# Performance work log

Hardware: AMD Instinct MI355X
Metric: run time of the kernel (lower is better)

The kernel has to match this reference:

```python
import jax, jax.numpy as jnp
import numpy as np

N_NODES = 40000
N_EDGES = 640000
FEAT_IN = 128
EDGE_FEAT_IN = 16
HID = 128
N_LAYERS = 4
NUM_GRAPHS = 256


def _linear_params(key, fan_in, fan_out):
    k1, k2 = jax.random.split(key)
    s = 1.0 / np.sqrt(fan_in)
    W = jax.random.uniform(k1, (fan_in, fan_out), jnp.float32, -s, s)
    b = jax.random.uniform(k2, (fan_out,), jnp.float32, -s, s)
    return W, b


def setup_inputs() -> dict:
    key = jax.random.key(0)
    ks = jax.random.split(key, 8)
    h = jax.random.normal(ks[0], (N_NODES, FEAT_IN), jnp.float32)
    e = jax.random.normal(ks[1], (N_EDGES, EDGE_FEAT_IN), jnp.float32)
    edge_index = jax.random.randint(ks[2], (2, N_EDGES), 0, N_NODES, jnp.int32)
    batch = jnp.sort(jax.random.randint(ks[3], (N_NODES,), 0, NUM_GRAPHS, jnp.int32))

    W_embed, b_embed = _linear_params(ks[4], FEAT_IN, HID)
    W_eembed, b_eembed = _linear_params(ks[5], EDGE_FEAT_IN, HID)

    layer_keys = jax.random.split(ks[6], N_LAYERS * 3)
    Wm_l, bm_l, Wh_l, bh_l, We_l, be_l = [], [], [], [], [], []
    for i in range(N_LAYERS):
        Wm, bm = _linear_params(layer_keys[3 * i + 0], 3 * HID, HID)
        Wh, bh = _linear_params(layer_keys[3 * i + 1], 2 * HID, HID)
        We, be = _linear_params(layer_keys[3 * i + 2], 3 * HID, HID)
        Wm_l.append(Wm); bm_l.append(bm)
        Wh_l.append(Wh); bh_l.append(bh)
        We_l.append(We); be_l.append(be)

    return {
        "h": h, "e": e, "edge_index": edge_index, "batch": batch,
        "W_embed": W_embed, "b_embed": b_embed,
        "W_eembed": W_eembed, "b_eembed": b_eembed,
        "Wm": jnp.stack(Wm_l), "bm": jnp.stack(bm_l),
        "Wh": jnp.stack(Wh_l), "bh": jnp.stack(bh_l),
        "We": jnp.stack(We_l), "be": jnp.stack(be_l),
    }


def reference(h, e, W_embed, b_embed, W_eembed, b_eembed,
              Wm, bm, Wh, bh, We, be, edge_index, batch):
    send, rec = edge_index[0], edge_index[1]
    h = h @ W_embed + b_embed          # [N, H]
    e = e @ W_eembed + b_eembed        # [E, H]

    def layer(carry, params):
        h, e = carry
        Wm_i, bm_i, Wh_i, bh_i, We_i, be_i = params
        h_send = h[send]               # [E, H] gather
        h_rec = h[rec]                 # [E, H] gather
        cat3 = jnp.concatenate([h_send, h_rec, e], axis=1)  # [E, 3H]
        messages = cat3 @ Wm_i + bm_i                        # [E, H]
        agg = jax.ops.segment_sum(messages, rec, num_segments=N_NODES)  # scatter_add
        h_new = jnp.concatenate([h, agg], axis=1) @ Wh_i + bh_i
        # NOTE: e_update uses h_send/h_rec from the OLD h, as in the source.
        e_new = cat3 @ We_i + be_i
        return (h_new, e_new), None

    (h, e), _ = jax.lax.scan(layer, (h, e), (Wm, bm, Wh, bh, We, be))
    return jax.ops.segment_sum(h, batch, num_segments=NUM_GRAPHS)  # global_add_pool
```

## Files before the change

kernel.cpp:

```cpp
#include <hip/hip_runtime.h>
#include <hip/hip_bf16.h>

#define NN 40000
#define NE 640000
#define NG 256
#define EW 48

typedef __attribute__((ext_vector_type(8))) short bf16x8;
typedef __attribute__((ext_vector_type(4))) float f32x4;

__device__ __forceinline__ unsigned f2b_u(float f){
  unsigned u = __builtin_bit_cast(unsigned, f);
  u += 0x7fffu + ((u >> 16) & 1u);
  return u >> 16;
}
__device__ __forceinline__ float b2f(unsigned short h){
  unsigned u = ((unsigned)h) << 16;
  return __builtin_bit_cast(float, u);
}
__device__ __forceinline__ unsigned scale_pk(unsigned u, float dg){
  float lo = __builtin_bit_cast(float, u << 16);
  float hi = __builtin_bit_cast(float, u & 0xffff0000u);
  return f2b_u(lo * dg) | (f2b_u(hi * dg) << 16);
}

#define LSTRIDE 147456

__global__ __launch_bounds__(256) void pack2_k(
    const float* __restrict__ Wembed, const float* __restrict__ Wh,
    const float* __restrict__ We, unsigned short* __restrict__ wt,
    unsigned short* __restrict__ wp)
{
  __shared__ float T[64][65];
  const int bx = blockIdx.x;
  const int tx = threadIdx.x & 63, ty = threadIdx.x >> 6;
  const float* src; unsigned short* dst; int rowbase, stride, koff, jt, kt;
  if (bx < 4){
    src = Wembed; dst = wt; rowbase = 0; stride = 128; koff = 0;
    kt = bx & 1; jt = bx >> 1;
  } else {
    const int q = bx - 4, l = q / 24, w = q % 24;
    unsigned short* base = wt + 16384 + (size_t)l * LSTRIDE;
    const float* wh = Wh + (size_t)l * 256 * 128;
    const float* we = We + (size_t)l * 384 * 128;
    if (w < 4){       src = wh; rowbase = 0;   dst = base;          stride = 640; koff = 0;   kt = w & 1;        jt = w >> 1; }
    else if (w < 12){ const int u = w - 4;  src = we; rowbase = 128; dst = base + 81920;  stride = 256; koff = 0;   kt = u & 3; jt = u >> 2; }
    else if (w < 16){ const int u = w - 12; src = we; rowbase = 0;   dst = base + 114688; stride = 256; koff = 0;   kt = u & 1; jt = u >> 1; }
    else if (w < 20){ const int u = w - 16; src = we; rowbase = 256; dst = base + 114688; stride = 256; koff = 128; kt = u & 1; jt = u >> 1; }
    else {            const int u = w - 20; src = wh; rowbase = 128; dst = wp + l * 16384; stride = 128; koff = 0; kt = u & 1; jt = u >> 1; }
  }
  const int k0 = kt * 64, j0 = jt * 64;
  #pragma unroll
  for (int rr = 0; rr < 16; ++rr){
    const int r = ty + rr * 4;
    T[r][tx] = src[(size_t)(rowbase + k0 + r) * 128 + j0 + tx];
  }
  __syncthreads();
  #pragma unroll
  for (int rr = 0; rr < 16; ++rr){
    const int j = ty + rr * 4;
    dst[(size_t)(j0 + j) * stride + koff + k0 + tx] = (unsigned short)f2b_u(T[tx][j]);
  }
}

__global__ __launch_bounds__(256, 2) void prodg_k(
    const float* __restrict__ Wm, const unsigned short* __restrict__ wp,
    unsigned short* __restrict__ wt)
{
  __shared__ unsigned short As[128 * 128];
  __shared__ unsigned short Bs[128 * 128];
  const int l = blockIdx.x / 3, pi = blockIdx.x % 3;
  const int rowoff = (pi == 0) ? 128 : (pi == 1) ? 0 : 256;
  const int poff   = (pi == 0) ? 128 : (pi == 1) ? 256 : 384;
  const float* Am = Wm + (size_t)l * 384 * 128 + (size_t)rowoff * 128;
  const unsigned short* Bt = wp + l * 16384;
  unsigned short* base = wt + 16384 + (size_t)l * LSTRIDE;

  const int tid = threadIdx.x;
  const int lane = tid & 63, wave = tid >> 6;
  const int qm = (wave & 1) << 6, qn = (wave >> 1) << 6;
  const int lr = lane & 15, lkc = lane >> 4;
  const int chunk = tid & 15, r0 = tid >> 4;
  f32x4 acc[4][4] = {};

  #pragma unroll
  for (int rr = 0; rr < 8; ++rr){
    const int r = r0 + rr * 16;
    const float* Af = Am + ((size_t)r << 7) + chunk * 8;
    const float4 f0 = *(const float4*)Af;
    const float4 f1 = *(const float4*)(Af + 4);
    uint4 va;
    va.x = f2b_u(f0.x) | (f2b_u(f0.y) << 16);
    va.y = f2b_u(f0.z) | (f2b_u(f0.w) << 16);
    va.z = f2b_u(f1.x) | (f2b_u(f1.y) << 16);
    va.w = f2b_u(f1.z) | (f2b_u(f1.w) << 16);
    *(uint4*)&As[r * 128 + ((chunk ^ (r & 7)) << 3)] = va;
    *(uint4*)&Bs[r * 128 + ((chunk ^ (r & 7)) << 3)] =
        *(const uint4*)(Bt + (size_t)r * 128 + chunk * 8);
  }
  __syncthreads();
  #pragma unroll
  for (int kk = 0; kk < 4; ++kk){
    const int kc = kk * 4 + lkc;
    bf16x8 af[4], bfr[4];
    #pragma unroll
    for (int mi = 0; mi < 4; ++mi){
      const int r = qm + mi * 16 + lr;
      af[mi] = *(const bf16x8*)&As[r * 128 + ((kc ^ (r & 7)) << 3)];
    }
    #pragma unroll
    for (int ni = 0; ni < 4; ++ni){
      const int r = qn + ni * 16 + lr;
      bfr[ni] = *(const bf16x8*)&Bs[r * 128 + ((kc ^ (r & 7)) << 3)];
    }
    #pragma unroll
    for (int mi = 0; mi < 4; ++mi)
      #pragma unroll
      for (int ni = 0; ni < 4; ++ni)
        acc[mi][ni] = __builtin_amdgcn_mfma_f32_16x16x32_bf16(af[mi], bfr[ni], acc[mi][ni], 0, 0, 0);
  }

  const int rbase = (lane >> 4) << 2;
  #pragma unroll
  for (int mi = 0; mi < 4; ++mi){
    #pragma unroll
    for (int r = 0; r < 4; ++r){
      const int gr = qm + mi * 16 + rbase + r;
      #pragma unroll
      for (int ni = 0; ni < 4; ++ni){
        const int col = qn + ni * 16 + lr;
        const unsigned short b = (unsigned short)f2b_u(acc[mi][ni][r]);
        base[(size_t)col * 640 + poff + gr] = b;
        if (pi == 2) base[(size_t)col * 640 + 512 + gr] = b;
      }
    }
  }
}

__global__ __launch_bounds__(1024, 1) void vec2b_k(
    const float* __restrict__ bm, const float* __restrict__ be,
    const unsigned short* __restrict__ wt, const unsigned short* __restrict__ wp,
    float* __restrict__ rw)
{
  __shared__ unsigned short s_wp[16384];
  __shared__ unsigned short s_m3[16384];
  __shared__ unsigned short s_w3[16384];
  __shared__ float c[128], cb[128];
  __shared__ float part_rw[128][8], part_cn[128][8];
  const int t = threadIdx.x;
  const int j = t >> 3, p = t & 7;
  if (t < 128) c[t] = 0.f;

  for (int l = 0; l < 4; ++l){
    const unsigned short* base = wt + 16384 + (size_t)l * LSTRIDE;
    ((uint4*)s_wp)[t]        = ((const uint4*)(wp + l * 16384))[t];
    ((uint4*)s_wp)[t + 1024] = ((const uint4*)(wp + l * 16384))[t + 1024];
    {
      const uint4* srcm = (const uint4*)(base + (size_t)j * 640 + 384);
      ((uint4*)(s_m3 + j * 128))[p * 2]     = srcm[p * 2];
      ((uint4*)(s_m3 + j * 128))[p * 2 + 1] = srcm[p * 2 + 1];
      const uint4* srcw = (const uint4*)(base + 114688 + (size_t)j * 256 + 128);
      ((uint4*)(s_w3 + j * 128))[p * 2]     = srcw[p * 2];
      ((uint4*)(s_w3 + j * 128))[p * 2 + 1] = srcw[p * 2 + 1];
    }
    if (t < 128) cb[t] = bm[l * 128 + t];
    __syncthreads();
    float prw = 0.f, pcn = 0.f;
    #pragma unroll
    for (int q = 0; q < 16; ++q){
      const int kk = p * 16 + q;
      prw += cb[kk] * b2f(s_wp[j * 128 + kk]) + c[kk] * b2f(s_m3[j * 128 + kk]);
      pcn += c[kk] * b2f(s_w3[j * 128 + kk]);
    }
    part_rw[j][p] = prw; part_cn[j][p] = pcn;
    __syncthreads();
    if (t < 128){
      float rwj = 0.f, cnj = be[l * 128 + t];
      #pragma unroll
      for (int i = 0; i < 8; ++i){ rwj += part_rw[t][i]; cnj += part_cn[t][i]; }
      rw[l * 128 + t] = rwj;
      __syncthreads();
      c[t] = cnj;
    } else {
      __syncthreads();
    }
    __syncthreads();
  }
}

struct YCfg {
  const void* A[5];
  const unsigned short* Bt;
  unsigned short* out0;
  const float* bias;
  const float* rv;
  int np;
  int bstride;
  int scale_mask;
};
struct GArgs { YCfg y[3]; };

template<int AT0>
__global__ __launch_bounds__(256, 2) void gemm_multi(
    GArgs ga, int M, const float* __restrict__ degf)
{
  __shared__ unsigned short As[128 * 128];
  __shared__ unsigned short Bs[128 * 128];
  const YCfg c = ga.y[blockIdx.y];
  const int tid = threadIdx.x;
  const int m0 = blockIdx.x * 128;
  const int lane = tid & 63, wave = tid >> 6;
  const int qm = (wave & 1) << 6, qn = (wave >> 1) << 6;
  const int lr = lane & 15, lkc = lane >> 4;
  const int chunk = tid & 15, r0 = tid >> 4;
  f32x4 acc[4][4] = {};

  for (int p = 0; p < c.np; ++p){
    if (p) __syncthreads();
    const unsigned short* Ab = (const unsigned short*)c.A[p];
    const bool scl = (c.scale_mask >> p) & 1;
    #pragma unroll
    for (int rr = 0; rr < 8; ++rr){
      const int r = r0 + rr * 16;
      const int gr = m0 + r;
      uint4 va = make_uint4(0u, 0u, 0u, 0u);
      if (gr < M){
        if (AT0 && p == 0){
          const float* Af = (const float*)c.A[0] + ((size_t)gr << 7) + chunk * 8;
          const float4 f0 = *(const float4*)Af;
          const float4 f1 = *(const float4*)(Af + 4);
          va.x = f2b_u(f0.x) | (f2b_u(f0.y) << 16);
          va.y = f2b_u(f0.z) | (f2b_u(f0.w) << 16);
          va.z = f2b_u(f1.x) | (f2b_u(f1.y) << 16);
          va.w = f2b_u(f1.z) | (f2b_u(f1.w) << 16);
        } else {
          va = *(const uint4*)(Ab + ((size_t)gr << 7) + chunk * 8);
          if (scl){
            const float dg = degf[gr];
            va.x = scale_pk(va.x, dg); va.y = scale_pk(va.y, dg);
            va.z = scale_pk(va.z, dg); va.w = scale_pk(va.w, dg);
          }
        }
      }
      *(uint4*)&As[r * 128 + ((chunk ^ (r & 7)) << 3)] = va;
      *(uint4*)&Bs[r * 128 + ((chunk ^ (r & 7)) << 3)] =
          *(const uint4*)(c.Bt + (size_t)r * c.bstride + p * 128 + chunk * 8);
    }
    __syncthreads();
    #pragma unroll
    for (int kk = 0; kk < 4; ++kk){
      const int kc = kk * 4 + lkc;
      bf16x8 af[4], bfr[4];
      #pragma unroll
      for (int mi = 0; mi < 4; ++mi){
        const int r = qm + mi * 16 + lr;
        af[mi] = *(const bf16x8*)&As[r * 128 + ((kc ^ (r & 7)) << 3)];
      }
      #pragma unroll
      for (int ni = 0; ni < 4; ++ni){
        const int r = qn + ni * 16 + lr;
        bfr[ni] = *(const bf16x8*)&Bs[r * 128 + ((kc ^ (r & 7)) << 3)];
      }
      #pragma unroll
      for (int mi = 0; mi < 4; ++mi)
        #pragma unroll
        for (int ni = 0; ni < 4; ++ni)
          acc[mi][ni] = __builtin_amdgcn_mfma_f32_16x16x32_bf16(af[mi], bfr[ni], acc[mi][ni], 0, 0, 0);
    }
  }

  const int rbase = (lane >> 4) << 2;
  #pragma unroll
  for (int mi = 0; mi < 4; ++mi){
    #pragma unroll
    for (int r = 0; r < 4; ++r){
      const int gr = m0 + qm + mi * 16 + rbase + r;
      if (gr >= M) continue;
      const size_t ro = (size_t)gr << 7;
      float dg = 0.f;
      if (c.rv) dg = degf[gr];
      #pragma unroll
      for (int ni = 0; ni < 4; ++ni){
        const int col = qn + ni * 16 + lr;
        float v = acc[mi][ni][r];
        if (c.bias) v += c.bias[col];
        if (c.rv)   v += dg * c.rv[col];
        c.out0[ro + col] = (unsigned short)f2b_u(v);
      }
    }
  }
}

__global__ void fill_ell_k(const int* __restrict__ rec, const int* __restrict__ send,
                           int* __restrict__ cnt, int* __restrict__ ell_s,
                           int* __restrict__ ell_e){
  const int i = blockIdx.x * 256 + threadIdx.x;
  if (i < NE){
    const int r = rec[i];
    const int k = atomicAdd(&cnt[r], 1);
    if (k < EW){
      ell_s[r * EW + k] = send[i];
      ell_e[r * EW + k] = i;
    }
  }
}

__global__ void aux_k(const int* __restrict__ cnt, float* __restrict__ degf,
                      const int* __restrict__ batch, int* __restrict__ gptr){
  const int b = blockIdx.x, t = threadIdx.x;
  if (b < 157){
    const int i = b * 256 + t;
    if (i < NN) degf[i] = (float)cnt[i];
  } else {
    if (t < NG){
      int lo = 0, hi = NN;
      while (lo < hi){
        const int mid = (lo + hi) >> 1;
        if (batch[mid] < t) lo = mid + 1; else hi = mid;
      }
      gptr[t] = lo;
      if (t == 0) gptr[NG] = NN;
    }
  }
}

__global__ __launch_bounds__(256) void sraw_s0_k(
    const int* __restrict__ cnt, const int* __restrict__ ell_e,
    const float* __restrict__ e_in, const float* __restrict__ W,
    const float* __restrict__ bias, unsigned short* __restrict__ TPS)
{
  __shared__ float sums[16][16];
  __shared__ float dgs[16];
  __shared__ float Ws[2048];
  __shared__ float bs[128];
  const int t = threadIdx.x;
  const int n0 = blockIdx.x * 16;
  for (int i = t; i < 2048; i += 256) Ws[i] = W[i];
  if (t < 128) bs[t] = bias[t];
  {
    const int a = t >> 4, c16 = t & 15;
    const int n = n0 + a;
    const int m0 = cnt[n];
    const int m = (m0 < EW) ? m0 : EW;
    const int* row = ell_e + n * EW;
    float acc = 0.f;
    int j = 0;
    for (; j + 2 <= m; j += 2){
      const int e0 = row[j], e1 = row[j + 1];
      acc += e_in[(size_t)e0 * 16 + c16] + e_in[(size_t)e1 * 16 + c16];
    }
    if (j < m) acc += e_in[(size_t)row[j] * 16 + c16];
    sums[a][c16] = acc;
    if (c16 == 0) dgs[a] = (float)m0;
  }
  __syncthreads();
  #pragma unroll
  for (int i = 0; i < 8; ++i){
    const int o = t + 256 * i;
    const int node = o >> 7, col = o & 127;
    float acc = dgs[node] * bs[col];
    #pragma unroll
    for (int k = 0; k < 16; ++k) acc += sums[node][k] * Ws[k * 128 + col];
    TPS[((size_t)(n0 + node) << 7) + col] = (unsigned short)f2b_u(acc);
  }
}

__global__ __launch_bounds__(256) void gather_k(
    const int* __restrict__ cnt, const int* __restrict__ ell_s,
    const unsigned short* __restrict__ hb, unsigned short* __restrict__ tb)
{
  const int n = blockIdx.x * 4 + (threadIdx.x >> 6);
  const int lane = threadIdx.x & 63;
  const int half = lane >> 5, l32 = lane & 31;
  const int mc = cnt[n];
  const int m = (mc < EW) ? mc : EW;
  const unsigned short* colp = hb + 4 * l32;
  const int myidx = (lane < m) ? ell_s[n * EW + lane] : 0;
  float a0 = 0.f, a1 = 0.f, a2 = 0.f, a3 = 0.f;
  int k = 0;
  for (; k + 16 <= m; k += 16){
    int s[8];
    #pragma unroll
    for (int u = 0; u < 8; ++u) s[u] = __shfl(myidx, k + 2 * u + half);
    uint2 v[8];
    #pragma unroll
    for (int u = 0; u < 8; ++u) v[u] = *(const uint2*)(colp + ((size_t)s[u] << 7));
    #pragma unroll
    for (int u = 0; u < 8; ++u){
      a0 += b2f((unsigned short)(v[u].x & 0xffffu));
      a1 += b2f((unsigned short)(v[u].x >> 16));
      a2 += b2f((unsigned short)(v[u].y & 0xffffu));
      a3 += b2f((unsigned short)(v[u].y >> 16));
    }
  }
  for (; k + 4 <= m; k += 4){
    const int s0 = __shfl(myidx, k + half);
    const int s1 = __shfl(myidx, k + 2 + half);
    const uint2 v0 = *(const uint2*)(colp + ((size_t)s0 << 7));
    const uint2 v1 = *(const uint2*)(colp + ((size_t)s1 << 7));
    a0 += b2f((unsigned short)(v0.x & 0xffffu)) + b2f((unsigned short)(v1.x & 0xffffu));
    a1 += b2f((unsigned short)(v0.x >> 16)) + b2f((unsigned short)(v1.x >> 16));
    a2 += b2f((unsigned short)(v0.y & 0xffffu)) + b2f((unsigned short)(v1.y & 0xffffu));
    a3 += b2f((unsigned short)(v0.y >> 16)) + b2f((unsigned short)(v1.y >> 16));
  }
  for (; k < m; k += 2){
    if (k + half < m){
      const int s = __shfl(myidx, k + half);
      const uint2 v = *(const uint2*)(colp + ((size_t)s << 7));
      a0 += b2f((unsigned short)(v.x & 0xffffu));
      a1 += b2f((unsigned short)(v.x >> 16));
      a2 += b2f((unsigned short)(v.y & 0xffffu));
      a3 += b2f((unsigned short)(v.y >> 16));
    }
  }
  a0 += __shfl_xor(a0, 32); a1 += __shfl_xor(a1, 32);
  a2 += __shfl_xor(a2, 32); a3 += __shfl_xor(a3, 32);
  if (half == 0){
    uint2 o;
    o.x = f2b_u(a0) | (f2b_u(a1) << 16);
    o.y = f2b_u(a2) | (f2b_u(a3) << 16);
    *(uint2*)(tb + ((size_t)n << 7) + 4 * l32) = o;
  }
}

__global__ void pool_k(const int* __restrict__ gptr, const unsigned short* __restrict__ hb,
                       float* __restrict__ out)
{
  const int g = blockIdx.x * 4 + (threadIdx.x >> 6);
  const int lane = threadIdx.x & 63;
  float a0 = 0.f, a1 = 0.f;
  for (int n = gptr[g]; n < gptr[g + 1]; ++n){
    const unsigned v = *(const unsigned*)(hb + ((size_t)n << 7) + 2 * lane);
    a0 += b2f((unsigned short)(v & 0xffffu));
    a1 += b2f((unsigned short)(v >> 16));
  }
  float2 r; r.x = a0; r.y = a1;
  *(float2*)(out + (size_t)g * 128 + 2 * lane) = r;
}

extern "C" void kernel_launch(void* const* d_in, const int* in_sizes, int n_in,
                              void* d_out, int out_size, void* d_ws, size_t ws_size,
                              hipStream_t stream)
{
  const float* h_in     = (const float*)d_in[0];
  const float* e_in     = (const float*)d_in[1];
  const int*   eidx     = (const int*)d_in[2];
  const int*   batch    = (const int*)d_in[3];
  const float* W_embed  = (const float*)d_in[4];
  const float* b_embed  = (const float*)d_in[5];
  const float* W_eembed = (const float*)d_in[6];
  const float* b_eembed = (const float*)d_in[7];
  const float* Wm       = (const float*)d_in[8];
  const float* bm       = (const float*)d_in[9];
  const float* Wh       = (const float*)d_in[10];
  const float* bh       = (const float*)d_in[11];
  const float* We       = (const float*)d_in[12];
  const float* be       = (const float*)d_in[13];
  const int* send = eidx;
  const int* rec  = eidx + NE;

  char* ws = (char*)d_ws;
  size_t off = 0;
  auto alloc = [&](size_t bytes) -> char* {
    char* p = ws + off;
    off = (off + bytes + 255) & ~(size_t)255;
    return p;
  };
  unsigned short* wt  = (unsigned short*)alloc((size_t)(16384 + 4 * LSTRIDE) * 2);
  unsigned short* wp  = (unsigned short*)alloc((size_t)4 * 16384 * 2);
  unsigned short* hA  = (unsigned short*)alloc((size_t)NN * 128 * 2);
  unsigned short* hB  = (unsigned short*)alloc((size_t)NN * 128 * 2);
  unsigned short* Q0  = (unsigned short*)alloc((size_t)NN * 128 * 2);
  unsigned short* Q1  = (unsigned short*)alloc((size_t)NN * 128 * 2);
  unsigned short* T0  = (unsigned short*)alloc((size_t)NN * 128 * 2);
  unsigned short* T1  = (unsigned short*)alloc((size_t)NN * 128 * 2);
  unsigned short* tb  = (unsigned short*)alloc((size_t)NN * 128 * 2);
  float* rw   = (float*)alloc((size_t)512 * 4);
  int* cnt    = (int*)alloc((size_t)NN * 4);
  float* degf = (float*)alloc((size_t)NN * 4);
  int* gptr   = (int*)alloc((size_t)(NG + 1) * 4);
  int* ell_s  = (int*)alloc((size_t)NN * EW * 4);
  int* ell_e  = (int*)tb;

  if (off > ws_size) return;

  const dim3 B256(256);

  pack2_k<<<dim3(100), B256, 0, stream>>>(W_embed, Wh, We, wt, wp);
  prodg_k<<<dim3(12), B256, 0, stream>>>(Wm, wp, wt);
  vec2b_k<<<dim3(1), dim3(1024), 0, stream>>>(bm, be, wt, wp, rw);

  hipMemsetAsync(cnt, 0, (size_t)NN * 4, stream);
  fill_ell_k<<<dim3(2500), B256, 0, stream>>>(rec, send, cnt, ell_s, ell_e);
  aux_k<<<dim3(158), B256, 0, stream>>>(cnt, degf, batch, gptr);
  sraw_s0_k<<<dim3(NN / 16), B256, 0, stream>>>(cnt, ell_e, e_in, W_eembed, b_eembed, T0);

  {
    GArgs ga = {};
    ga.y[0].A[0] = h_in; ga.y[0].Bt = wt; ga.y[0].out0 = hA;
    ga.y[0].bias = b_embed; ga.y[0].np = 1; ga.y[0].bstride = 128;
    ga.y[0].scale_mask = 0;
    gemm_multi<1><<<dim3(313, 1), B256, 0, stream>>>(ga, NN, degf);
  }

  unsigned short* hc = hA;  unsigned short* hn = hB;
  unsigned short* Qc = Q0;  unsigned short* Qn = Q1;
  unsigned short* Tc = T0;  unsigned short* Tn = T1;
  for (int l = 0; l < 4; ++l){
    const unsigned short* LB = wt + 16384 + (size_t)l * LSTRIDE;

    gather_k<<<dim3(NN / 4), B256, 0, stream>>>(cnt, ell_s, hc, tb);

    GArgs ga = {};
    YCfg& y0 = ga.y[0];
    y0.A[0] = hc; y0.A[1] = hc; y0.A[2] = tb; y0.A[3] = Tc; y0.A[4] = Qc;
    y0.Bt = LB; y0.out0 = hn; y0.bias = bh + l * 128; y0.rv = rw + l * 128;
    y0.np = (l == 0) ? 4 : 5;
    y0.bstride = 640; y0.scale_mask = (1 << 1) | (1 << 4);
    int ny = 1;
    if (l < 3){
      YCfg& y1 = ga.y[1];
      y1.A[0] = hc; y1.A[1] = Qc; y1.Bt = LB + 81920;
      y1.out0 = Qn; y1.np = (l == 0) ? 1 : 2; y1.bstride = 256; y1.scale_mask = 0;
      YCfg& y2 = ga.y[2];
      y2.A[0] = tb; y2.A[1] = Tc; y2.Bt = LB + 114688;
      y2.out0 = Tn; y2.np = 2; y2.bstride = 256; y2.scale_mask = 0;
      ny = 3;
    }
    gemm_multi<0><<<dim3(313, ny), B256, 0, stream>>>(ga, NN, degf);

    unsigned short* t2;
    t2 = hc; hc = hn; hn = t2;
    t2 = Qc; Qc = Qn; Qn = t2;
    t2 = Tc; Tc = Tn; Tn = t2;
  }

  pool_k<<<dim3(NG / 4), B256, 0, stream>>>(gptr, hc, (float*)d_out);
}
```

Baseline: 599.4 us.

## Pre-fragment weights and load B operands directly from global memory in GEMM

Adds a kernel that rearranges the packed bf16 weight matrices into an MFMA-fragment-friendly layout, one 16K-element block per K-slice. The GEMM then reads B fragments straight from global/L2 instead of staging them through shared memory. This halves LDS usage and raises launch bounds to allow four blocks per SM. The trade-off is that every wave re-reads the weight fragments from cache on each k-step, which adds global load latency inside the MFMA loop.

```diff
diff --git a/kernel.cpp b/kernel.cpp
--- a/kernel.cpp
+++ b/kernel.cpp
@@ -137,6 +137,26 @@
   }
 }
 
+__global__ void frag_k(const unsigned short* __restrict__ wt,
+                       unsigned short* __restrict__ wf)
+{
+  const int gp = blockIdx.y;
+  const int g = blockIdx.x * 256 + threadIdx.x;
+  const int kc = g >> 7, r = g & 127;
+  const unsigned short* src; unsigned short* dst; int bstride, p;
+  if (gp == 0){ src = wt; dst = wf; bstride = 128; p = 0; }
+  else {
+    const int q = gp - 1, l = q / 9, w = q % 9;
+    const unsigned short* sb = wt + 16384 + (size_t)l * LSTRIDE;
+    dst = wf + 16384 + (size_t)l * LSTRIDE + w * 16384;
+    if (w < 5){      src = sb;           bstride = 640; p = w; }
+    else if (w < 7){ src = sb + 81920;   bstride = 256; p = w - 5; }
+    else {           src = sb + 114688;  bstride = 256; p = w - 7; }
+  }
+  *(uint4*)(dst + (size_t)g * 8) =
+      *(const uint4*)(src + (size_t)r * bstride + p * 128 + kc * 8);
+}
+
 __global__ __launch_bounds__(1024, 1) void vec2b_k(
     const float* __restrict__ bm, const float* __restrict__ be,
     const unsigned short* __restrict__ wt, const unsigned short* __restrict__ wp,
@@ -190,22 +210,21 @@
 
 struct YCfg {
   const void* A[5];
-  const unsigned short* Bt;
+  int bo[5];
   unsigned short* out0;
   const float* bias;
   const float* rv;
   int np;
-  int bstride;
   int scale_mask;
 };
 struct GArgs { YCfg y[3]; };
 
 template<int AT0>
-__global__ __launch_bounds__(256, 2) void gemm_multi(
-    GArgs ga, int M, const float* __restrict__ degf)
+__global__ __launch_bounds__(256, 4) void gemm_multi(
+    GArgs ga, int M, const float* __restrict__ degf,
+    const unsigned short* __restrict__ wf)
 {
   __shared__ unsigned short As[128 * 128];
-  __shared__ unsigned short Bs[128 * 128];
   const YCfg c = ga.y[blockIdx.y];
   const int tid = threadIdx.x;
   const int m0 = blockIdx.x * 128;
@@ -243,23 +262,20 @@
         }
       }
       *(uint4*)&As[r * 128 + ((chunk ^ (r & 7)) << 3)] = va;
-      *(uint4*)&Bs[r * 128 + ((chunk ^ (r & 7)) << 3)] =
-          *(const uint4*)(c.Bt + (size_t)r * c.bstride + p * 128 + chunk * 8);
     }
     __syncthreads();
     #pragma unroll
     for (int kk = 0; kk < 4; ++kk){
       const int kc = kk * 4 + lkc;
-      bf16x8 af[4], bfr[4];
+      const bf16x8* bp = (const bf16x8*)(wf + c.bo[p]) + (size_t)kc * 128 + qn + lr;
+      bf16x8 bfr[4];
+      #pragma unroll
+      for (int ni = 0; ni < 4; ++ni) bfr[ni] = bp[ni * 16];
+      bf16x8 af[4];
       #pragma unroll
       for (int mi = 0; mi < 4; ++mi){
         const int r = qm + mi * 16 + lr;
         af[mi] = *(const bf16x8*)&As[r * 128 + ((kc ^ (r & 7)) << 3)];
-      }
-      #pragma unroll
-      for (int ni = 0; ni < 4; ++ni){
-        const int r = qn + ni * 16 + lr;
-        bfr[ni] = *(const bf16x8*)&Bs[r * 128 + ((kc ^ (r & 7)) << 3)];
       }
       #pragma unroll
       for (int mi = 0; mi < 4; ++mi)
@@ -467,6 +483,7 @@
     return p;
   };
   unsigned short* wt  = (unsigned short*)alloc((size_t)(16384 + 4 * LSTRIDE) * 2);
+  unsigned short* wf  = (unsigned short*)alloc((size_t)(16384 + 4 * LSTRIDE) * 2);
   unsigned short* wp  = (unsigned short*)alloc((size_t)4 * 16384 * 2);
   unsigned short* hA  = (unsigned short*)alloc((size_t)NN * 128 * 2);
   unsigned short* hB  = (unsigned short*)alloc((size_t)NN * 128 * 2);
@@ -488,6 +505,7 @@
 
   pack2_k<<<dim3(100), B256, 0, stream>>>(W_embed, Wh, We, wt, wp);
   prodg_k<<<dim3(12), B256, 0, stream>>>(Wm, wp, wt);
+  frag_k<<<dim3(8, 37), B256, 0, stream>>>(wt, wf);
   vec2b_k<<<dim3(1), dim3(1024), 0, stream>>>(bm, be, wt, wp, rw);
 
   hipMemsetAsync(cnt, 0, (size_t)NN * 4, stream);
@@ -497,37 +515,46 @@
 
   {
     GArgs ga = {};
-    ga.y[0].A[0] = h_in; ga.y[0].Bt = wt; ga.y[0].out0 = hA;
-    ga.y[0].bias = b_embed; ga.y[0].np = 1; ga.y[0].bstride = 128;
-    ga.y[0].scale_mask = 0;
-    gemm_multi<1><<<dim3(313, 1), B256, 0, stream>>>(ga, NN, degf);
+    YCfg& y = ga.y[0];
+    y.A[0] = h_in; y.bo[0] = 0;
+    y.out0 = hA; y.bias = b_embed; y.rv = nullptr;
+    y.np = 1; y.scale_mask = 0;
+    gemm_multi<1><<<dim3(313, 1), B256, 0, stream>>>(ga, NN, degf, wf);
   }
 
   unsigned short* hc = hA;  unsigned short* hn = hB;
   unsigned short* Qc = Q0;  unsigned short* Qn = Q1;
   unsigned short* Tc = T0;  unsigned short* Tn = T1;
   for (int l = 0; l < 4; ++l){
-    const unsigned short* LB = wt + 16384 + (size_t)l * LSTRIDE;
+    const int LB = 16384 + l * LSTRIDE;
 
     gather_k<<<dim3(NN / 4), B256, 0, stream>>>(cnt, ell_s, hc, tb);
 
     GArgs ga = {};
     YCfg& y0 = ga.y[0];
-    y0.A[0] = hc; y0.A[1] = hc; y0.A[2] = tb; y0.A[3] = Tc; y0.A[4] = Qc;
-    y0.Bt = LB; y0.out0 = hn; y0.bias = bh + l * 128; y0.rv = rw + l * 128;
+    y0.A[0] = hc; y0.bo[0] = LB;
+    y0.A[1] = hc; y0.bo[1] = LB + 16384;
+    y0.A[2] = tb; y0.bo[2] = LB + 32768;
+    y0.A[3] = Tc; y0.bo[3] = LB + 49152;
+    y0.A[4] = Qc; y0.bo[4] = LB + 65536;
+    y0.out0 = hn; y0.bias = bh + l * 128; y0.rv = rw + l * 128;
     y0.np = (l == 0) ? 4 : 5;
-    y0.bstride = 640; y0.scale_mask = (1 << 1) | (1 << 4);
+    y0.scale_mask = (1 << 1) | (1 << 4);
     int ny = 1;
     if (l < 3){
       YCfg& y1 = ga.y[1];
-      y1.A[0] = hc; y1.A[1] = Qc; y1.Bt = LB + 81920;
-      y1.out0 = Qn; y1.np = (l == 0) ? 1 : 2; y1.bstride = 256; y1.scale_mask = 0;
+      y1.A[0] = hc; y1.bo[0] = LB + 81920;
+      y1.A[1] = Qc; y1.bo[1] = LB + 98304;
+      y1.out0 = Qn; y1.bias = nullptr; y1.rv = nullptr;
+      y1.np = (l == 0) ? 1 : 2; y1.scale_mask = 0;
       YCfg& y2 = ga.y[2];
-      y2.A[0] = tb; y2.A[1] = Tc; y2.Bt = LB + 114688;
-      y2.out0 = Tn; y2.np = 2; y2.bstride = 256; y2.scale_mask = 0;
+      y2.A[0] = tb; y2.bo[0] = LB + 114688;
+      y2.A[1] = Tc; y2.bo[1] = LB + 131072;
+      y2.out0 = Tn; y2.bias = nullptr; y2.rv = nullptr;
+      y2.np = 2; y2.scale_mask = 0;
       ny = 3;
     }
-    gemm_multi<0><<<dim3(313, ny), B256, 0, stream>>>(ga, NN, degf);
+    gemm_multi<0><<<dim3(313, ny), B256, 0, stream>>>(ga, NN, degf, wf);
 
     unsigned short* t2;
     t2 = hc; hc = hn; hn = t2;
```

Result: slower. 631.0 us (+5.3%).
